# Performance work log

Hardware: AMD Instinct MI355X
Metric: run time of the kernel (lower is better)

Reference implementation:

```python
import jax, jax.numpy as jnp
import numpy as np

TEMPERATURE = 0.1
USE_RANKS = True
USE_SCORES = True
RANK_WEIGHT = 0.1
SCORE_WEIGHT = 0.01
NUM_GROUPS = 1024  # question_ids in [0, NUM_GROUPS)
BATCH = 4096
DIM = 1024


def setup_inputs() -> dict:
    key = jax.random.key(0)
    k1, k2, k3, k4, k5 = jax.random.split(key, 5)
    q_embeddings = jax.random.normal(k1, (BATCH, DIM), dtype=jnp.float32)
    a_embeddings = jax.random.normal(k2, (BATCH, DIM), dtype=jnp.float32)
    question_ids = jax.random.randint(k3, (BATCH,), 0, NUM_GROUPS, dtype=jnp.int32)
    ranks = jax.random.uniform(k4, (BATCH,), dtype=jnp.float32) * 8.0  # ordinal-ish ranks
    scores = jax.random.uniform(k5, (BATCH,), dtype=jnp.float32)
    return {
        "q_embeddings": q_embeddings,
        "a_embeddings": a_embeddings,
        "question_ids": question_ids,
        "ranks": ranks,
        "scores": scores,
    }


def _positive_weights(question_ids, ranks, scores):
    """Per-sample positive weight, normalized to sum to 1 within each question group."""
    w = jnp.ones_like(ranks)
    if USE_RANKS:
        w = w * jnp.exp(-RANK_WEIGHT * ranks)
    if USE_SCORES:
        gmax = jax.ops.segment_max(scores, question_ids, num_segments=NUM_GROUPS)
        gmin = jax.ops.segment_min(scores, question_ids, num_segments=NUM_GROUPS)
        denom = gmax[question_ids] - gmin[question_ids]
        norm = jnp.where(denom > 0, (scores - gmin[question_ids]) / jnp.where(denom > 0, denom, 1.0), 0.0)
        w = w * jnp.exp(SCORE_WEIGHT * norm)
    wsum = jax.ops.segment_sum(w, question_ids, num_segments=NUM_GROUPS)[question_ids]
    gsize = jax.ops.segment_sum(jnp.ones_like(w), question_ids, num_segments=NUM_GROUPS)[question_ids]
    w = jnp.where(wsum > 0, w / jnp.where(wsum > 0, wsum, 1.0), 1.0 / gsize)
    return w


def reference(q_embeddings, a_embeddings, question_ids, ranks, scores):
    B = q_embeddings.shape[0]
    # [B, B] similarity, one fused batched log-softmax over rows
    similarity = jnp.matmul(q_embeddings, a_embeddings.T) / TEMPERATURE
    log_probs = jax.nn.log_softmax(similarity, axis=1)
    # same-group mask: sample j is a positive for row i iff same question id
    same = (question_ids[:, None] == question_ids[None, :])
    w = _positive_weights(question_ids, ranks, scores)  # [B], group-normalized
    # loss_i = -sum_{j in group(i)} w_j * log_probs[i, j]; total averaged over batch
    per_row = -jnp.sum(jnp.where(same, w[None, :] * log_probs, 0.0), axis=1)
    loss = jnp.sum(per_row) / B
    # accuracy: argmax of each row lands inside the row's group
    pred = jnp.argmax(similarity, axis=1)
    acc = jnp.mean((question_ids[pred] == question_ids).astype(jnp.float32))
    return loss, acc
```

## Files before the change

kernel.cpp:

```cpp
#include <hip/hip_runtime.h>
#include <hip/hip_bf16.h>
#include <math.h>

#define BATCH   4096
#define DIM     1024
#define NGROUPS 1024
#define INV_T   10.0f
#define RANK_W  0.1f
#define SCORE_W 0.01f

#define BI 128
#define BJ 256
#define KC 32
#define NT (DIM/KC)
#define NFRAG_Q (BI/16)
#define NFRAG   (BI/16 + BJ/16)
#define NSTG    3
#define FRAG_ELEMS 512

typedef float  floatx4 __attribute__((ext_vector_type(4)));
typedef __bf16 bf16x8  __attribute__((ext_vector_type(8)));
typedef __bf16 bf16x4  __attribute__((ext_vector_type(4)));

#define ASYNC_COPY16(gptr, lptr)                                              \
    __builtin_amdgcn_global_load_lds(                                         \
        (const __attribute__((address_space(1))) void*)(gptr),                \
        (__attribute__((address_space(3))) void*)(lptr), 16, 0, 0)

__global__ __launch_bounds__(256) void prep_kernel(
    const float* __restrict__ Q, const float* __restrict__ A,
    __bf16* __restrict__ Qb, __bf16* __restrict__ Ab,
    const int* __restrict__ qid, const float* __restrict__ ranks,
    const float* __restrict__ scores, float* __restrict__ w)
{
    const int tid = threadIdx.x;

    if (blockIdx.x >= NGROUPS) {
        const int cid = blockIdx.x - NGROUPS;
        const int n4  = BATCH * DIM / 4;
        for (int i = cid * 256 + tid; i < n4; i += 1024 * 256) {
            float4 v = ((const float4*)Q)[i];
            bf16x4 b;
            b[0] = (__bf16)v.x; b[1] = (__bf16)v.y;
            b[2] = (__bf16)v.z; b[3] = (__bf16)v.w;
            ((bf16x4*)Qb)[i] = b;
            v = ((const float4*)A)[i];
            b[0] = (__bf16)v.x; b[1] = (__bf16)v.y;
            b[2] = (__bf16)v.z; b[3] = (__bf16)v.w;
            ((bf16x4*)Ab)[i] = b;
        }
        return;
    }

    const int g = blockIdx.x, lane = tid & 63, wv = tid >> 6;
    __shared__ float rmax[4], rmin[4], rsum[4];

    float gmax = -INFINITY, gmin = INFINITY;
    for (int j = tid; j < BATCH; j += 256) {
        if (qid[j] == g) {
            float s = scores[j];
            gmax = fmaxf(gmax, s);
            gmin = fminf(gmin, s);
        }
    }
    #pragma unroll
    for (int d = 1; d < 64; d <<= 1) {
        gmax = fmaxf(gmax, __shfl_xor(gmax, d, 64));
        gmin = fminf(gmin, __shfl_xor(gmin, d, 64));
    }
    if (lane == 0) { rmax[wv] = gmax; rmin[wv] = gmin; }
    __syncthreads();
    gmax = fmaxf(fmaxf(rmax[0], rmax[1]), fmaxf(rmax[2], rmax[3]));
    gmin = fminf(fminf(rmin[0], rmin[1]), fminf(rmin[2], rmin[3]));
    const float denom     = gmax - gmin;
    const float inv_denom = (denom > 0.f) ? 1.f / denom : 0.f;

    float lsum = 0.f;
    for (int j = tid; j < BATCH; j += 256) {
        if (qid[j] == g) {
            float norm = (scores[j] - gmin) * inv_denom;
            float u = __expf(-RANK_W * ranks[j] + SCORE_W * norm);
            w[j] = u;
            lsum += u;
        }
    }
    #pragma unroll
    for (int d = 1; d < 64; d <<= 1) lsum += __shfl_xor(lsum, d, 64);
    if (lane == 0) rsum[wv] = lsum;
    __syncthreads();
    const float wsum = rsum[0] + rsum[1] + rsum[2] + rsum[3];
    const float inv  = (wsum > 0.f) ? 1.f / wsum : 0.f;
    for (int j = tid; j < BATCH; j += 256) {
        if (qid[j] == g) w[j] *= inv;
    }
}

__global__ __launch_bounds__(512, 4) void fused_simloss_kernel(
    const __bf16* __restrict__ Qb, const __bf16* __restrict__ Ab,
    const int* __restrict__ qid, const float* __restrict__ w,
    float* __restrict__ Pm, float* __restrict__ Pl, float* __restrict__ Ps,
    float* __restrict__ Pbv, int* __restrict__ Pbi)
{
    __shared__ __bf16 sbuf[3][NFRAG * FRAG_ELEMS];

    const int jb = blockIdx.x, ib = blockIdx.y;
    const int i0 = ib * BI, j0 = jb * BJ;
    const int tid = threadIdx.x, wid = tid >> 6, lane = tid & 63;
    const int wm = wid >> 2, wn = wid & 3;
    const int quad = lane >> 4, l16 = lane & 15;

    floatx4 acc[4][4];
    #pragma unroll
    for (int m = 0; m < 4; ++m)
        #pragma unroll
        for (int n = 0; n < 4; ++n)
            #pragma unroll
            for (int c = 0; c < 4; ++c) acc[m][n][c] = 0.f;

    const int lr = lane & 15;
    const int lk = (lane >> 4) * 8;
    const __bf16* src[NSTG];
    #pragma unroll
    for (int c = 0; c < NSTG; ++c) {
        const int f = wid * NSTG + c;
        src[c] = (f < NFRAG_Q)
               ? Qb + (size_t)(i0 + f * 16 + lr) * DIM + lk
               : Ab + (size_t)(j0 + (f - NFRAG_Q) * 16 + lr) * DIM + lk;
    }

    #define STAGE(bufptr, k0)                                                 \
        do {                                                                  \
            _Pragma("unroll")                                                 \
            for (int c = 0; c < NSTG; ++c)                                    \
                ASYNC_COPY16(src[c] + (k0),                                   \
                             (__bf16*)(bufptr) + (wid * NSTG + c) * FRAG_ELEMS); \
        } while (0)

    __bf16* bprev = sbuf[2];
    __bf16* bcur  = sbuf[0];
    __bf16* bnext = sbuf[1];

    STAGE(bcur, 0);
    STAGE(bnext, KC);

    for (int t = 0; t < NT; ++t) {
        if (t < NT - 1) asm volatile("s_waitcnt vmcnt(3)\n\ts_barrier" ::: "memory");
        else            asm volatile("s_waitcnt vmcnt(0)\n\ts_barrier" ::: "memory");

        if (t + 2 < NT) STAGE(bprev, (t + 2) * KC);

        const __bf16* cur = bcur;
        bf16x8 qf[4], af[4];
        #pragma unroll
        for (int mf = 0; mf < 4; ++mf)
            qf[mf] = *(const bf16x8*)&cur[(wm * 4 + mf) * FRAG_ELEMS + lane * 8];
        #pragma unroll
        for (int nf = 0; nf < 4; ++nf)
            af[nf] = *(const bf16x8*)&cur[(NFRAG_Q + wn * 4 + nf) * FRAG_ELEMS + lane * 8];

        __builtin_amdgcn_s_setprio(1);
        #pragma unroll
        for (int nf = 0; nf < 4; ++nf)
            #pragma unroll
            for (int mf = 0; mf < 4; ++mf)
                acc[mf][nf] = __builtin_amdgcn_mfma_f32_16x16x32_bf16(
                    qf[mf], af[nf], acc[mf][nf], 0, 0, 0);
        __builtin_amdgcn_s_setprio(0);

        __bf16* tmp = bprev;
        bprev = bcur; bcur = bnext; bnext = tmp;
    }
    #undef STAGE

    int cq[4]; float cw[4];
    #pragma unroll
    for (int n = 0; n < 4; ++n) {
        int col = j0 + wn * 64 + n * 16 + l16;
        cq[n] = qid[col];
        cw[n] = w[col];
    }
    const int slice = jb * 4 + wn;

    #pragma unroll
    for (int m = 0; m < 4; ++m) {
        #pragma unroll
        for (int reg = 0; reg < 4; ++reg) {
            const int row = i0 + wm * 64 + m * 16 + quad * 4 + reg;
            const int rq  = qid[row];

            float v[4];
            #pragma unroll
            for (int n = 0; n < 4; ++n) v[n] = acc[m][n][reg] * INV_T;

            float pm = fmaxf(fmaxf(v[0], v[1]), fmaxf(v[2], v[3]));
            #pragma unroll
            for (int d = 1; d < 16; d <<= 1)
                pm = fmaxf(pm, __shfl_xor(pm, d, 64));

            float ll = __expf(v[0] - pm) + __expf(v[1] - pm) +
                       __expf(v[2] - pm) + __expf(v[3] - pm);
            float ls = 0.f;
            #pragma unroll
            for (int n = 0; n < 4; ++n) ls += (cq[n] == rq) ? cw[n] * v[n] : 0.f;

            float bv = v[0];
            int   bi = j0 + wn * 64 + l16;
            #pragma unroll
            for (int n = 1; n < 4; ++n) {
                int c = j0 + wn * 64 + n * 16 + l16;
                if (v[n] > bv) { bv = v[n]; bi = c; }
            }

            #pragma unroll
            for (int d = 1; d < 16; d <<= 1) {
                ll += __shfl_xor(ll, d, 64);
                ls += __shfl_xor(ls, d, 64);
                float obv = __shfl_xor(bv, d, 64);
                int   obi = __shfl_xor(bi, d, 64);
                if (obv > bv || (obv == bv && obi < bi)) { bv = obv; bi = obi; }
            }
            if (l16 == 0) {
                int idx = row * 64 + slice;
                Pm[idx] = pm; Pl[idx] = ll; Ps[idx] = ls;
                Pbv[idx] = bv; Pbi[idx] = bi;
            }
        }
    }
}

__global__ __launch_bounds__(256) void row_reduce_kernel(
    const float* __restrict__ Pm, const float* __restrict__ Pl,
    const float* __restrict__ Ps, const float* __restrict__ Pbv,
    const int* __restrict__ Pbi, const int* __restrict__ qid,
    float* __restrict__ per_row, float* __restrict__ ind)
{
    const int r    = blockIdx.x * 4 + (threadIdx.x >> 6);
    const int lane = threadIdx.x & 63;
    const int idx  = r * 64 + lane;

    float m = Pm[idx], l = Pl[idx], s = Ps[idx], bv = Pbv[idx];
    int   bi = Pbi[idx];

    #pragma unroll
    for (int d = 1; d < 64; d <<= 1) {
        float om  = __shfl_xor(m, d, 64);
        float ol  = __shfl_xor(l, d, 64);
        float os  = __shfl_xor(s, d, 64);
        float obv = __shfl_xor(bv, d, 64);
        int   obi = __shfl_xor(bi, d, 64);
        float nm = fmaxf(m, om);
        l = l * __expf(m - nm) + ol * __expf(om - nm);
        m = nm;
        s += os;
        if (obv > bv || (obv == bv && obi < bi)) { bv = obv; bi = obi; }
    }
    if (lane == 0) {
        per_row[r] = (m + logf(l)) - s;
        ind[r]     = (qid[bi] == qid[r]) ? 1.f : 0.f;
    }
}

__global__ __launch_bounds__(1024) void final_kernel(
    const float* __restrict__ per_row, const float* __restrict__ ind,
    float* __restrict__ out)
{
    const int tid = threadIdx.x;
    float s1 = 0.f, s2 = 0.f;
    for (int i = tid; i < BATCH; i += 1024) { s1 += per_row[i]; s2 += ind[i]; }
    #pragma unroll
    for (int d = 1; d < 64; d <<= 1) {
        s1 += __shfl_xor(s1, d, 64);
        s2 += __shfl_xor(s2, d, 64);
    }
    __shared__ float r1[16], r2[16];
    if ((tid & 63) == 0) { r1[tid >> 6] = s1; r2[tid >> 6] = s2; }
    __syncthreads();
    if (tid == 0) {
        float t1 = 0.f, t2 = 0.f;
        #pragma unroll
        for (int i = 0; i < 16; ++i) { t1 += r1[i]; t2 += r2[i]; }
        out[0] = t1 / (float)BATCH;
        out[1] = t2 / (float)BATCH;
    }
}

extern "C" void kernel_launch(void* const* d_in, const int* in_sizes, int n_in,
                              void* d_out, int out_size, void* d_ws, size_t ws_size,
                              hipStream_t stream)
{
    const float* Q      = (const float*)d_in[0];
    const float* A      = (const float*)d_in[1];
    const int*   qid    = (const int*)d_in[2];
    const float* ranks  = (const float*)d_in[3];
    const float* scores = (const float*)d_in[4];
    float* out = (float*)d_out;

    __bf16* Qb = (__bf16*)d_ws;
    __bf16* Ab = Qb + (size_t)BATCH * DIM;
    float* w       = (float*)(Ab + (size_t)BATCH * DIM);
    float* Pm      = w + BATCH;
    float* Pl      = Pm + BATCH * 64;
    float* Ps      = Pl + BATCH * 64;
    float* Pbv     = Ps + BATCH * 64;
    int*   Pbi     = (int*)(Pbv + BATCH * 64);
    float* per_row = (float*)(Pbi + BATCH * 64);
    float* ind     = per_row + BATCH;

    prep_kernel<<<2048, 256, 0, stream>>>(Q, A, Qb, Ab, qid, ranks, scores, w);

    dim3 grid(BATCH / BJ, BATCH / BI);
    fused_simloss_kernel<<<grid, 512, 0, stream>>>(Qb, Ab, qid, w, Pm, Pl, Ps, Pbv, Pbi);

    row_reduce_kernel<<<BATCH / 4, 256, 0, stream>>>(Pm, Pl, Ps, Pbv, Pbi, qid, per_row, ind);

    final_kernel<<<1, 1024, 0, stream>>>(per_row, ind, out);
}
```

Before: 157.0 us.

## Fuse row and final reductions into GEMM kernel via last-block atomic counter

Removes the separate row_reduce and final kernels. Each row-block of the fused similarity kernel increments a per-row-block counter after a threadfence. The last-arriving column block reduces the 64 partials per row and atomically adds the scaled loss and accuracy sums into the output. Counters and output are zeroed in the prep kernel. This saves two kernel launches and a round trip through per_row/ind, at the cost of atomics, float atomic nondeterminism, and a serial tail in the last blocks.

```diff
diff --git a/kernel.cpp b/kernel.cpp
--- a/kernel.cpp
+++ b/kernel.cpp
@@ -17,6 +17,7 @@
 #define NFRAG   (BI/16 + BJ/16)
 #define NSTG    3
 #define FRAG_ELEMS 512
+#define NJB     (BATCH/BJ)
 
 typedef float  floatx4 __attribute__((ext_vector_type(4)));
 typedef __bf16 bf16x8  __attribute__((ext_vector_type(8)));
@@ -31,7 +32,8 @@
     const float* __restrict__ Q, const float* __restrict__ A,
     __bf16* __restrict__ Qb, __bf16* __restrict__ Ab,
     const int* __restrict__ qid, const float* __restrict__ ranks,
-    const float* __restrict__ scores, float* __restrict__ w)
+    const float* __restrict__ scores, float* __restrict__ w,
+    float* __restrict__ out, int* __restrict__ cnt)
 {
     const int tid = threadIdx.x;
 
@@ -53,6 +55,12 @@
     }
 
     const int g = blockIdx.x, lane = tid & 63, wv = tid >> 6;
+
+    if (g == 0) {
+        if (tid < 2)  out[tid] = 0.f;
+        if (tid < BATCH / BI) cnt[tid] = 0;
+    }
+
     __shared__ float rmax[4], rmin[4], rsum[4];
 
     float gmax = -INFINITY, gmin = INFINITY;
@@ -99,9 +107,11 @@
     const __bf16* __restrict__ Qb, const __bf16* __restrict__ Ab,
     const int* __restrict__ qid, const float* __restrict__ w,
     float* __restrict__ Pm, float* __restrict__ Pl, float* __restrict__ Ps,
-    float* __restrict__ Pbv, int* __restrict__ Pbi)
+    float* __restrict__ Pbv, int* __restrict__ Pbi,
+    int* __restrict__ cnt, float* __restrict__ out)
 {
     __shared__ __bf16 sbuf[3][NFRAG * FRAG_ELEMS];
+    __shared__ int last_flag;
 
     const int jb = blockIdx.x, ib = blockIdx.y;
     const int i0 = ib * BI, j0 = jb * BJ;
@@ -226,61 +236,45 @@
             }
         }
     }
-}
-
-__global__ __launch_bounds__(256) void row_reduce_kernel(
-    const float* __restrict__ Pm, const float* __restrict__ Pl,
-    const float* __restrict__ Ps, const float* __restrict__ Pbv,
-    const int* __restrict__ Pbi, const int* __restrict__ qid,
-    float* __restrict__ per_row, float* __restrict__ ind)
-{
-    const int r    = blockIdx.x * 4 + (threadIdx.x >> 6);
-    const int lane = threadIdx.x & 63;
-    const int idx  = r * 64 + lane;
-
-    float m = Pm[idx], l = Pl[idx], s = Ps[idx], bv = Pbv[idx];
-    int   bi = Pbi[idx];
-
-    #pragma unroll
-    for (int d = 1; d < 64; d <<= 1) {
-        float om  = __shfl_xor(m, d, 64);
-        float ol  = __shfl_xor(l, d, 64);
-        float os  = __shfl_xor(s, d, 64);
-        float obv = __shfl_xor(bv, d, 64);
-        int   obi = __shfl_xor(bi, d, 64);
-        float nm = fmaxf(m, om);
-        l = l * __expf(m - nm) + ol * __expf(om - nm);
-        m = nm;
-        s += os;
-        if (obv > bv || (obv == bv && obi < bi)) { bv = obv; bi = obi; }
-    }
-    if (lane == 0) {
-        per_row[r] = (m + logf(l)) - s;
-        ind[r]     = (qid[bi] == qid[r]) ? 1.f : 0.f;
-    }
-}
-
-__global__ __launch_bounds__(1024) void final_kernel(
-    const float* __restrict__ per_row, const float* __restrict__ ind,
-    float* __restrict__ out)
-{
-    const int tid = threadIdx.x;
-    float s1 = 0.f, s2 = 0.f;
-    for (int i = tid; i < BATCH; i += 1024) { s1 += per_row[i]; s2 += ind[i]; }
-    #pragma unroll
-    for (int d = 1; d < 64; d <<= 1) {
-        s1 += __shfl_xor(s1, d, 64);
-        s2 += __shfl_xor(s2, d, 64);
-    }
-    __shared__ float r1[16], r2[16];
-    if ((tid & 63) == 0) { r1[tid >> 6] = s1; r2[tid >> 6] = s2; }
+
+    __threadfence();
     __syncthreads();
     if (tid == 0) {
-        float t1 = 0.f, t2 = 0.f;
-        #pragma unroll
-        for (int i = 0; i < 16; ++i) { t1 += r1[i]; t2 += r2[i]; }
-        out[0] = t1 / (float)BATCH;
-        out[1] = t2 / (float)BATCH;
+        int prev = atomicAdd(&cnt[ib], 1);
+        last_flag = (prev == NJB - 1) ? 1 : 0;
+    }
+    __syncthreads();
+    if (!last_flag) return;
+
+    __threadfence();
+
+    float s1 = 0.f, s2 = 0.f;
+    for (int rr = wid; rr < BI; rr += 8) {
+        const int row = i0 + rr;
+        const int idx = row * 64 + lane;
+        float m = Pm[idx], l = Pl[idx], s = Ps[idx], bv = Pbv[idx];
+        int   bi = Pbi[idx];
+        #pragma unroll
+        for (int d = 1; d < 64; d <<= 1) {
+            float om  = __shfl_xor(m, d, 64);
+            float ol  = __shfl_xor(l, d, 64);
+            float os  = __shfl_xor(s, d, 64);
+            float obv = __shfl_xor(bv, d, 64);
+            int   obi = __shfl_xor(bi, d, 64);
+            float nm = fmaxf(m, om);
+            l = l * __expf(m - nm) + ol * __expf(om - nm);
+            m = nm;
+            s += os;
+            if (obv > bv || (obv == bv && obi < bi)) { bv = obv; bi = obi; }
+        }
+        if (lane == 0) {
+            s1 += (m + logf(l)) - s;
+            s2 += (qid[bi] == qid[row]) ? 1.f : 0.f;
+        }
+    }
+    if (lane == 0) {
+        atomicAdd(&out[0], s1 * (1.f / (float)BATCH));
+        atomicAdd(&out[1], s2 * (1.f / (float)BATCH));
     }
 }
 
@@ -297,21 +291,19 @@
 
     __bf16* Qb = (__bf16*)d_ws;
     __bf16* Ab = Qb + (size_t)BATCH * DIM;
-    float* w       = (float*)(Ab + (size_t)BATCH * DIM);
-    float* Pm      = w + BATCH;
-    float* Pl      = Pm + BATCH * 64;
-    float* Ps      = Pl + BATCH * 64;
-    float* Pbv     = Ps + BATCH * 64;
-    int*   Pbi     = (int*)(Pbv + BATCH * 64);
-    float* per_row = (float*)(Pbi + BATCH * 64);
-    float* ind     = per_row + BATCH;
-
-    prep_kernel<<<2048, 256, 0, stream>>>(Q, A, Qb, Ab, qid, ranks, scores, w);
+    float* w   = (float*)(Ab + (size_t)BATCH * DIM);
+    float* Pm  = w + BATCH;
+    float* Pl  = Pm + BATCH * 64;
+    float* Ps  = Pl + BATCH * 64;
+    float* Pbv = Ps + BATCH * 64;
+    int*   Pbi = (int*)(Pbv + BATCH * 64);
+    int*   cnt = Pbi + BATCH * 64;
+
+    prep_kernel<<<2048, 256, 0, stream>>>(Q, A, Qb, Ab, qid, ranks, scores, w,
+                                          out, cnt);
 
     dim3 grid(BATCH / BJ, BATCH / BI);
-    fused_simloss_kernel<<<grid, 512, 0, stream>>>(Qb, Ab, qid, w, Pm, Pl, Ps, Pbv, Pbi);
-
-    row_reduce_kernel<<<BATCH / 4, 256, 0, stream>>>(Pm, Pl, Ps, Pbv, Pbi, qid, per_row, ind);
-
-    final_kernel<<<1, 1024, 0, stream>>>(per_row, ind, out);
+    fused_simloss_kernel<<<grid, 512, 0, stream>>>(Qb, Ab, qid, w,
+                                                   Pm, Pl, Ps, Pbv, Pbi,
+                                                   cnt, out);
 }
```

Measured after the change: 329.9 us. +110.1%, slower.

## Compute group weights in one block via LDS atomics; fuse final reduction

Applied to the files above, without the earlier changes.

The per-group weight computation, which before ran as 1024 blocks each scanning the full batch, becomes a single block that stages ids and scores in LDS and uses shared-memory atomics for group max, min and sum. The final reduction kernel is removed: row_reduce accumulates the loss and accuracy into the output with global atomics, and prep zeroes the output first. This cuts redundant global scans and one launch. It relies on scores being non-negative so integer max/min on float bits orders correctly, and float atomics make the summation order nondeterministic.

```diff
diff --git a/kernel.cpp b/kernel.cpp
--- a/kernel.cpp
+++ b/kernel.cpp
@@ -31,12 +31,14 @@
     const float* __restrict__ Q, const float* __restrict__ A,
     __bf16* __restrict__ Qb, __bf16* __restrict__ Ab,
     const int* __restrict__ qid, const float* __restrict__ ranks,
-    const float* __restrict__ scores, float* __restrict__ w)
+    const float* __restrict__ scores, float* __restrict__ w,
+    float* __restrict__ out)
 {
     const int tid = threadIdx.x;
 
-    if (blockIdx.x >= NGROUPS) {
-        const int cid = blockIdx.x - NGROUPS;
+    if (blockIdx.x < 1024) {
+        if (blockIdx.x == 0 && tid < 2) out[tid] = 0.f;
+        const int cid = blockIdx.x;
         const int n4  = BATCH * DIM / 4;
         for (int i = cid * 256 + tid; i < n4; i += 1024 * 256) {
             float4 v = ((const float4*)Q)[i];
@@ -52,46 +54,56 @@
         return;
     }
 
-    const int g = blockIdx.x, lane = tid & 63, wv = tid >> 6;
-    __shared__ float rmax[4], rmin[4], rsum[4];
-
-    float gmax = -INFINITY, gmin = INFINITY;
-    for (int j = tid; j < BATCH; j += 256) {
-        if (qid[j] == g) {
-            float s = scores[j];
-            gmax = fmaxf(gmax, s);
-            gmin = fminf(gmin, s);
-        }
-    }
-    #pragma unroll
-    for (int d = 1; d < 64; d <<= 1) {
-        gmax = fmaxf(gmax, __shfl_xor(gmax, d, 64));
-        gmin = fminf(gmin, __shfl_xor(gmin, d, 64));
-    }
-    if (lane == 0) { rmax[wv] = gmax; rmin[wv] = gmin; }
+    __shared__ int   qidS[BATCH];
+    __shared__ float scoS[BATCH];
+    __shared__ int   gmaxS[NGROUPS];
+    __shared__ int   gminS[NGROUPS];
+    __shared__ float wsumS[NGROUPS];
+
+    #pragma unroll
+    for (int k = 0; k < BATCH / 256; ++k) {
+        const int j = tid + k * 256;
+        qidS[j] = qid[j];
+        scoS[j] = scores[j];
+    }
+    #pragma unroll
+    for (int k = 0; k < NGROUPS / 256; ++k) {
+        const int g = tid + k * 256;
+        gmaxS[g] = 0;
+        gminS[g] = 0x7F800000;
+        wsumS[g] = 0.f;
+    }
     __syncthreads();
-    gmax = fmaxf(fmaxf(rmax[0], rmax[1]), fmaxf(rmax[2], rmax[3]));
-    gmin = fminf(fminf(rmin[0], rmin[1]), fminf(rmin[2], rmin[3]));
-    const float denom     = gmax - gmin;
-    const float inv_denom = (denom > 0.f) ? 1.f / denom : 0.f;
-
-    float lsum = 0.f;
-    for (int j = tid; j < BATCH; j += 256) {
-        if (qid[j] == g) {
-            float norm = (scores[j] - gmin) * inv_denom;
-            float u = __expf(-RANK_W * ranks[j] + SCORE_W * norm);
-            w[j] = u;
-            lsum += u;
-        }
-    }
-    #pragma unroll
-    for (int d = 1; d < 64; d <<= 1) lsum += __shfl_xor(lsum, d, 64);
-    if (lane == 0) rsum[wv] = lsum;
+
+    #pragma unroll
+    for (int k = 0; k < BATCH / 256; ++k) {
+        const int j = tid + k * 256;
+        const int g = qidS[j];
+        const int sb = __float_as_int(scoS[j]);
+        atomicMax(&gmaxS[g], sb);
+        atomicMin(&gminS[g], sb);
+    }
     __syncthreads();
-    const float wsum = rsum[0] + rsum[1] + rsum[2] + rsum[3];
-    const float inv  = (wsum > 0.f) ? 1.f / wsum : 0.f;
-    for (int j = tid; j < BATCH; j += 256) {
-        if (qid[j] == g) w[j] *= inv;
+
+    float u[BATCH / 256];
+    #pragma unroll
+    for (int k = 0; k < BATCH / 256; ++k) {
+        const int j = tid + k * 256;
+        const int g = qidS[j];
+        const float gmax = __int_as_float(gmaxS[g]);
+        const float gmin = __int_as_float(gminS[g]);
+        const float d    = gmax - gmin;
+        const float invd = (d > 0.f) ? 1.f / d : 0.f;
+        const float norm = (scoS[j] - gmin) * invd;
+        u[k] = __expf(-RANK_W * ranks[j] + SCORE_W * norm);
+        atomicAdd(&wsumS[g], u[k]);
+    }
+    __syncthreads();
+
+    #pragma unroll
+    for (int k = 0; k < BATCH / 256; ++k) {
+        const int j = tid + k * 256;
+        w[j] = u[k] / wsumS[qidS[j]];
     }
 }
 
@@ -232,9 +244,10 @@
     const float* __restrict__ Pm, const float* __restrict__ Pl,
     const float* __restrict__ Ps, const float* __restrict__ Pbv,
     const int* __restrict__ Pbi, const int* __restrict__ qid,
-    float* __restrict__ per_row, float* __restrict__ ind)
+    float* __restrict__ out)
 {
-    const int r    = blockIdx.x * 4 + (threadIdx.x >> 6);
+    const int wv   = threadIdx.x >> 6;
+    const int r    = blockIdx.x * 4 + wv;
     const int lane = threadIdx.x & 63;
     const int idx  = r * 64 + lane;
 
@@ -254,33 +267,18 @@
         s += os;
         if (obv > bv || (obv == bv && obi < bi)) { bv = obv; bi = obi; }
     }
+
+    __shared__ float r1[4], r2[4];
     if (lane == 0) {
-        per_row[r] = (m + logf(l)) - s;
-        ind[r]     = (qid[bi] == qid[r]) ? 1.f : 0.f;
-    }
-}
-
-__global__ __launch_bounds__(1024) void final_kernel(
-    const float* __restrict__ per_row, const float* __restrict__ ind,
-    float* __restrict__ out)
-{
-    const int tid = threadIdx.x;
-    float s1 = 0.f, s2 = 0.f;
-    for (int i = tid; i < BATCH; i += 1024) { s1 += per_row[i]; s2 += ind[i]; }
-    #pragma unroll
-    for (int d = 1; d < 64; d <<= 1) {
-        s1 += __shfl_xor(s1, d, 64);
-        s2 += __shfl_xor(s2, d, 64);
-    }
-    __shared__ float r1[16], r2[16];
-    if ((tid & 63) == 0) { r1[tid >> 6] = s1; r2[tid >> 6] = s2; }
+        r1[wv] = (m + logf(l)) - s;
+        r2[wv] = (qid[bi] == qid[r]) ? 1.f : 0.f;
+    }
     __syncthreads();
-    if (tid == 0) {
-        float t1 = 0.f, t2 = 0.f;
-        #pragma unroll
-        for (int i = 0; i < 16; ++i) { t1 += r1[i]; t2 += r2[i]; }
-        out[0] = t1 / (float)BATCH;
-        out[1] = t2 / (float)BATCH;
+    if (threadIdx.x == 0) {
+        float t1 = r1[0] + r1[1] + r1[2] + r1[3];
+        float t2 = r2[0] + r2[1] + r2[2] + r2[3];
+        atomicAdd(&out[0], t1 * (1.f / (float)BATCH));
+        atomicAdd(&out[1], t2 * (1.f / (float)BATCH));
     }
 }
 
@@ -297,21 +295,17 @@
 
     __bf16* Qb = (__bf16*)d_ws;
     __bf16* Ab = Qb + (size_t)BATCH * DIM;
-    float* w       = (float*)(Ab + (size_t)BATCH * DIM);
-    float* Pm      = w + BATCH;
-    float* Pl      = Pm + BATCH * 64;
-    float* Ps      = Pl + BATCH * 64;
-    float* Pbv     = Ps + BATCH * 64;
-    int*   Pbi     = (int*)(Pbv + BATCH * 64);
-    float* per_row = (float*)(Pbi + BATCH * 64);
-    float* ind     = per_row + BATCH;
-
-    prep_kernel<<<2048, 256, 0, stream>>>(Q, A, Qb, Ab, qid, ranks, scores, w);
+    float* w   = (float*)(Ab + (size_t)BATCH * DIM);
+    float* Pm  = w + BATCH;
+    float* Pl  = Pm + BATCH * 64;
+    float* Ps  = Pl + BATCH * 64;
+    float* Pbv = Ps + BATCH * 64;
+    int*   Pbi = (int*)(Pbv + BATCH * 64);
+
+    prep_kernel<<<1025, 256, 0, stream>>>(Q, A, Qb, Ab, qid, ranks, scores, w, out);
 
     dim3 grid(BATCH / BJ, BATCH / BI);
     fused_simloss_kernel<<<grid, 512, 0, stream>>>(Qb, Ab, qid, w, Pm, Pl, Ps, Pbv, Pbi);
 
-    row_reduce_kernel<<<BATCH / 4, 256, 0, stream>>>(Pm, Pl, Ps, Pbv, Pbi, qid, per_row, ind);
-
-    final_kernel<<<1, 1024, 0, stream>>>(per_row, ind, out);
+    row_reduce_kernel<<<BATCH / 4, 256, 0, stream>>>(Pm, Pl, Ps, Pbv, Pbi, qid, out);
 }
```

After: 176.2 us. 12.2% more time.
